# Kernel optimization log

Hardware: AMD Instinct MI355X
Metric: run time of the kernel (lower is better)

The kernel has to match this reference:

```python
import jax, jax.numpy as jnp
import numpy as np

# module config (matches init_kwargs)
EMBED = 128; HEADS = 8; HEAD_DIM = EMBED // HEADS  # 16, power of 2
MODES = 16            # hardcoded in FuncSelfAttention
WS = 4                # window_size
SHIFT = 2             # shift_size
NSUB = 8              # n_sub (subdomain grid of the full image)
NW = (NSUB // WS) ** 2   # 4 windows per image
S = WS * WS              # 16 tokens (subdomains) per window
BATCH0 = 4; B = BATCH0 * NW  # 16
P = 32                # per-subdomain spatial resolution (needs P//2+1 >= MODES)
HID = 512             # LogCPB MLP hidden width (Swin-v2 style)


def win_decompose2d(x, nsx, nsy, ws):
    # x: [b, c, H, W] -> [(b*wx*wy), ws*ws, c, sh, sw]
    b, c, H, W = x.shape
    sh = H // nsx; sw = W // nsy
    wx = nsx // ws; wy = nsy // ws
    x = x.reshape(b, c, wx, ws, sh, wy, ws, sw)
    x = x.transpose(0, 2, 5, 3, 6, 1, 4, 7)  # b, wx, wy, qx, qy, c, sh, sw
    return x.reshape(b * wx * wy, ws * ws, c, sh, sw)


def win_recompose2d(x, nsx, nsy, ws):
    # inverse of win_decompose2d: [(b*wx*wy), ws*ws, c, sh, sw] -> [b, c, H, W]
    wx = nsx // ws; wy = nsy // ws
    Bn, s, c, sh, sw = x.shape
    b = Bn // (wx * wy)
    x = x.reshape(b, wx, wy, ws, ws, c, sh, sw)
    x = x.transpose(0, 5, 1, 3, 6, 2, 4, 7)
    return x.reshape(b, c, wx * ws * sh, wy * ws * sw)


def spectral_conv(x, wr, wi):
    # SimpleSpectralConv2d: rfft2 -> low-mode complex channel mixing -> irfft2
    # x: [b, s, cin, h, w]; wr/wi: [cin, cout, m, m]
    m = wr.shape[-1]
    h, w = x.shape[-2:]
    xf = jnp.fft.rfft2(x, axes=(-2, -1))                       # [b,s,cin,h,w//2+1]
    ym = jnp.einsum('bsixy,ioxy->bsoxy', xf[..., :m, :m], wr + 1j * wi)
    out_ft = jnp.zeros(x.shape[:2] + (wr.shape[1], h, w // 2 + 1), dtype=ym.dtype)
    out_ft = out_ft.at[..., :m, :m].set(ym)
    return jnp.fft.irfft2(out_ft, s=(h, w), axes=(-2, -1))


def log_cpb(ws, w1, b1, w2):
    # Swin-v2 style log-spaced continuous position bias MLP -> [heads, S, S]
    g = jnp.arange(ws)
    coords = jnp.stack(jnp.meshgrid(g, g, indexing='ij'), -1).reshape(-1, 2)  # [S,2]
    rel = (coords[:, None, :] - coords[None, :, :]).astype(jnp.float32)       # [S,S,2]
    rel = jnp.sign(rel) * jnp.log2(1.0 + jnp.abs(rel)) / jnp.log2(8.0) * 8.0
    hdn = jax.nn.relu(rel @ w1 + b1)
    return (hdn @ w2).transpose(2, 0, 1)


def _build_attn_mask():
    # Faithful port of the Swin shifted-window mask construction in __init__
    img = np.zeros((NSUB, NSUB), np.float32)
    sl = [slice(0, -WS), slice(-WS, -SHIFT), slice(-SHIFT, None)]
    cnt = 0
    for hs in sl:
        for ws_ in sl:
            img[hs, ws_] = cnt
            cnt += 1
    mw = img.reshape(NSUB // WS, WS, NSUB // WS, WS).transpose(0, 2, 1, 3).reshape(NW, S)
    diff = mw[:, None, :] - mw[:, :, None]
    m = np.where(diff != 0, -1e9, 0.0).astype(np.float32)      # -inf in torch; -1e9 for safe grads
    return np.broadcast_to(m[:, None, :, :], (NW, HEADS, S, S)).copy()


def setup_inputs():
    key = jax.random.key(0)
    ks = jax.random.split(key, 8)
    sc = 1.0 / EMBED
    return {
        'seq': jax.random.normal(ks[0], (B, S, EMBED, P, P), jnp.float32),
        'qkv_wr': jax.random.normal(ks[1], (EMBED, 3 * EMBED, MODES, MODES), jnp.float32) * sc,
        'qkv_wi': jax.random.normal(ks[2], (EMBED, 3 * EMBED, MODES, MODES), jnp.float32) * sc,
        'out_wr': jax.random.normal(ks[3], (EMBED, EMBED, MODES, MODES), jnp.float32) * sc,
        'out_wi': jax.random.normal(ks[4], (EMBED, EMBED, MODES, MODES), jnp.float32) * sc,
        'cpb_w1': jax.random.normal(ks[5], (2, HID), jnp.float32) * 0.1,
        'cpb_b1': jnp.zeros((HID,), jnp.float32),
        'cpb_w2': jax.random.normal(ks[6], (HID, HEADS), jnp.float32) * 0.05,
        'attn_mask': jnp.asarray(_build_attn_mask()),
    }


def reference(seq, qkv_wr, qkv_wi, out_wr, out_wi, cpb_w1, cpb_b1, cpb_w2, attn_mask):
    Bn, s, C, h, w = seq.shape
    ssx = w // WS; ssy = h // WS  # subdomain_size per code: seq.size(-1)//n_sub_x with n_sub_x=window_size
    # shift: recompose windows to images, roll, decompose back
    x = win_recompose2d(seq, WS, WS, WS)
    x = jnp.roll(x, (-SHIFT * ssx, -SHIFT * ssy), axis=(-2, -1))
    x = win_decompose2d(x, WS, WS, WS)
    # qkv = spectral conv + residual tiling (v.repeat with dims[2]=3)
    qkv = spectral_conv(x, qkv_wr, qkv_wi) + jnp.concatenate([x, x, x], axis=2)
    qkv = qkv.reshape(Bn, s, 3, HEADS, HEAD_DIM, h, w)
    q = qkv[:, :, 0].transpose(0, 2, 1, 3, 4, 5)  # [B, H, s, d, h, w]
    k = qkv[:, :, 1].transpose(0, 2, 1, 3, 4, 5)
    v = qkv[:, :, 2].transpose(0, 2, 1, 3, 4, 5)
    bias = attn_mask + log_cpb(WS, cpb_w1, cpb_b1, cpb_w2)[None]  # [nW, H, S, S]
    # 'reimann' scores: Riemann-sum (mean over grid) inner product of q_i, k_j functions
    scale = 1.0 / ((h * w) * jnp.sqrt(jnp.float32(HEAD_DIM)))
    scores = jnp.einsum('bnidxy,bnjdxy->bnij', q, k) * scale      # [B, H, S, S]
    scores = scores.reshape(Bn // NW, NW, HEADS, s, s) + bias[None]
    attn = jax.nn.softmax(scores, axis=-1).reshape(Bn, HEADS, s, s)
    sa = jnp.einsum('bnij,bnjdxy->bnidxy', attn, v)               # [B, H, S, d, h, w]
    sa = sa.transpose(0, 2, 1, 3, 4, 5).reshape(Bn, s, C, h, w)   # _flatten
    sa = spectral_conv(sa, out_wr, out_wi)
    # un-shift
    sa = win_recompose2d(sa, WS, WS, WS)
    sa = jnp.roll(sa, (SHIFT * ssx, SHIFT * ssy), axis=(-2, -1))
    return win_decompose2d(sa, WS, WS, WS)
```

## Files before the change

### kernel.cpp

```cpp
#include <hip/hip_runtime.h>
#include <hip/hip_bf16.h>
#include <math.h>


#define DEVI __device__ __forceinline__
typedef unsigned short u16;
typedef unsigned int u32;
typedef __attribute__((ext_vector_type(8))) short short8;
typedef __attribute__((ext_vector_type(4))) float f32x4;

DEVI u16 f2b(float f) {
  union { __hip_bfloat16 h; u16 u; } cv;
  cv.h = __float2bfloat16(f);
  return cv.u;
}
DEVI float b2f(u16 u) { return __uint_as_float(((u32)u) << 16); }

__global__ __launch_bounds__(256) void k_bias(
    const float* __restrict__ w1, const float* __restrict__ b1,
    const float* __restrict__ w2, const float* __restrict__ amask,
    float* __restrict__ biasb) {
  __shared__ float w1s[1024];
  __shared__ float b1s[512];
  __shared__ float w2s[4096];
  int t = threadIdx.x;
  for (int k = t; k < 1024; k += 256) w1s[k] = w1[k];
  for (int k = t; k < 512; k += 256) b1s[k] = b1[k];
  for (int k = t; k < 4096; k += 256) w2s[k] = w2[k];
  __syncthreads();
  int i = t >> 4, j = t & 15;
  float r0 = (float)((i >> 2) - (j >> 2));
  float r1 = (float)((i & 3) - (j & 3));
  const float sc = 8.0f / 3.0f;
  float f0 = (r0 == 0.f) ? 0.f : copysignf(log2f(1.f + fabsf(r0)) * sc, r0);
  float f1 = (r1 == 0.f) ? 0.f : copysignf(log2f(1.f + fabsf(r1)) * sc, r1);
  float o[8];
#pragma unroll
  for (int h = 0; h < 8; h++) o[h] = 0.f;
  for (int k = 0; k < 512; k++) {
    float hd = f0 * w1s[k] + f1 * w1s[512 + k] + b1s[k];
    hd = fmaxf(hd, 0.f);
#pragma unroll
    for (int h = 0; h < 8; h++) o[h] += hd * w2s[k * 8 + h];
  }
  for (int w = 0; w < 4; w++)
#pragma unroll
    for (int h = 0; h < 8; h++) {
      int idx = ((w * 8 + h) * 16 + i) * 16 + j;
      biasb[idx] = amask[idx] + o[h];
    }
}

__global__ __launch_bounds__(256) void k_transpose_wb(
    const float* __restrict__ wr, const float* __restrict__ wi,
    ushort2* __restrict__ dst, int N) {
  __shared__ ushort2 ld[256][17];
  int t = threadIdx.x;
  int ob = blockIdx.x * 16;
  int cb = blockIdx.y * 8;
  for (int cc = 0; cc < 8; cc++) {
    int c = cb + cc;
    for (int oo = 0; oo < 16; oo++) {
      size_t si = ((size_t)c * N + ob + oo) * 256 + t;
      ushort2 u;
      u.x = f2b(wr[si]);
      u.y = f2b(wi[si]);
      ld[t][oo] = u;
    }
    __syncthreads();
    {
      int oo = t & 15, tq = t >> 4;
#pragma unroll
      for (int mr = 0; mr < 16; mr++) {
        int m = mr * 16 + tq;
        dst[((size_t)m * 128 + c) * N + ob + oo] = ld[m][oo];
      }
    }
    __syncthreads();
  }
}

template <int N>
__global__ __launch_bounds__(256) void k_build_b(
    const ushort2* __restrict__ Ws1, u16* __restrict__ Bt) {
  __shared__ ushort2 tile[128][65];
  int t = threadIdx.x;
  int ob = blockIdx.x;
  int m = blockIdx.y;
  {
    int c4 = t >> 6, o = t & 63;
    for (int cc = 0; cc < 32; cc++) {
      int c = cc * 4 + c4;
      tile[c][o] = Ws1[((size_t)m * 128 + c) * N + ob * 64 + o];
    }
  }
  __syncthreads();
  int l = t & 63, w2 = t >> 6;
  for (int rr = 0; rr < 32; rr++) {
    int r = w2 * 32 + rr;
    int ol = r >> 1, p = r & 1;
    size_t rowoff = ((size_t)m * (2 * N) + (size_t)ob * 128 + r) * 256;
#pragma unroll
    for (int ch = 0; ch < 2; ch++) {
      int c = ch * 64 + l;
      ushort2 wv = tile[c][ol];
      ushort2 u;
      u.x = p ? wv.y : wv.x;
      u.y = p ? wv.x : (u16)(wv.y ^ 0x8000);
      *(ushort2*)(Bt + rowoff + 2 * c) = u;
    }
  }
}

__global__ __launch_bounds__(256) void k_build_wdft(u16* __restrict__ Wdft) {
  int n = blockIdx.x;
  int m = n >> 1, q = n & 1;
  int kx = m >> 4, ky = m & 15;
  int t = threadIdx.x;
#pragma unroll
  for (int i = 0; i < 4; i++) {
    int p = i * 256 + t;
    int u = p >> 5, v = p & 31;
    int ph = (kx * u + ky * v) & 31;
    float th = 6.283185307179586f * (float)ph / 32.f;
    float sv, cv;
    sincosf(th, &sv, &cv);
    Wdft[(size_t)n * 1024 + p] = f2b(q ? -sv : cv);
  }
}

__global__ __launch_bounds__(256) void k_gather(
    const float* __restrict__ seq, u16* __restrict__ Tbf) {
  int t = threadIdx.x;
  int cq = blockIdx.x;
  int bs = blockIdx.y;
  int b = bs >> 4, s = bs & 15;
  int qx = s >> 2, qy = s & 3;
  int u = t >> 3, vb = (t & 7) * 4;
  int uu = u + 16;
  int u2 = uu & 31;
  int qx2 = (qx + (uu >> 5)) & 3;
  int vv = vb + 16;
  int v2 = vv & 31;
  int qy2 = (qy + (vv >> 5)) & 3;
  int s2 = qx2 * 4 + qy2;
  size_t srcbase = (((size_t)(b * 16 + s2) * 128) << 10) + u2 * 32 + v2;
  size_t dstbase = (((size_t)bs * 128) << 10) + u * 32 + vb;
  for (int cc = 0; cc < 32; cc++) {
    size_t coff = (size_t)(cq * 32 + cc) << 10;
    float4 v = *(const float4*)(seq + srcbase + coff);
    ushort4 o;
    o.x = f2b(v.x);
    o.y = f2b(v.y);
    o.z = f2b(v.z);
    o.w = f2b(v.w);
    *(ushort4*)(Tbf + dstbase + coff) = o;
  }
}

__global__ __launch_bounds__(512) void k_dftm(
    const u16* __restrict__ Wdft, const u16* __restrict__ Tbf,
    float2* __restrict__ Xlow, u16* __restrict__ Xbf) {
  __shared__ char As[32768];
  __shared__ char Bs[16384];
  int t = threadIdx.x;
  int mt = blockIdx.x, bs = blockIdx.y;
  int l = t & 63, w = t >> 6;
  int wm = w >> 1, wn = w & 1;
  f32x4 acc[4][4];
#pragma unroll
  for (int a_ = 0; a_ < 4; a_++)
#pragma unroll
    for (int b_ = 0; b_ < 4; b_++) acc[a_][b_] = (f32x4){0.f, 0.f, 0.f, 0.f};
  const u16* Ab = Wdft + (size_t)mt * 256 * 1024;
  const u16* Bb = Tbf + (size_t)bs * 128 * 1024;
  int srow = t >> 3, ss = t & 7;
  uint4 ra[4], rb[2];
#pragma unroll
  for (int i = 0; i < 4; i++)
    ra[i] = *(const uint4*)(Ab + (size_t)(i * 64 + srow) * 1024 + ss * 8);
#pragma unroll
  for (int i = 0; i < 2; i++)
    rb[i] = *(const uint4*)(Bb + (size_t)(i * 64 + srow) * 1024 + ss * 8);
  for (int kt = 0; kt < 16; kt++) {
    if (kt) __syncthreads();
#pragma unroll
    for (int i = 0; i < 4; i++) {
      int row = i * 64 + srow;
      *(uint4*)(As + row * 128 + ((ss ^ (row & 7)) << 4)) = ra[i];
    }
#pragma unroll
    for (int i = 0; i < 2; i++) {
      int row = i * 64 + srow;
      *(uint4*)(Bs + row * 128 + ((ss ^ (row & 7)) << 4)) = rb[i];
    }
    if (kt < 15) {
#pragma unroll
      for (int i = 0; i < 4; i++)
        ra[i] = *(const uint4*)(Ab + (size_t)(i * 64 + srow) * 1024 +
                                (kt + 1) * 64 + ss * 8);
#pragma unroll
      for (int i = 0; i < 2; i++)
        rb[i] = *(const uint4*)(Bb + (size_t)(i * 64 + srow) * 1024 +
                                (kt + 1) * 64 + ss * 8);
    }
    __syncthreads();
#pragma unroll
    for (int kk = 0; kk < 2; kk++) {
      short8 af[4], bg[4];
#pragma unroll
      for (int fm = 0; fm < 4; fm++) {
        int row = wm * 64 + fm * 16 + (l & 15);
        int chunk = kk * 4 + (l >> 4);
        af[fm] = *(const short8*)(As + row * 128 + ((chunk ^ (row & 7)) << 4));
      }
#pragma unroll
      for (int fn = 0; fn < 4; fn++) {
        int row = wn * 64 + fn * 16 + (l & 15);
        int chunk = kk * 4 + (l >> 4);
        bg[fn] = *(const short8*)(Bs + row * 128 + ((chunk ^ (row & 7)) << 4));
      }
#pragma unroll
      for (int fm = 0; fm < 4; fm++)
#pragma unroll
        for (int fn = 0; fn < 4; fn++)
          acc[fm][fn] = __builtin_amdgcn_mfma_f32_16x16x32_bf16(
              af[fm], bg[fn], acc[fm][fn], 0, 0, 0);
    }
  }
  int cr = (l >> 4) * 4, ccol = l & 15;
#pragma unroll
  for (int fm = 0; fm < 4; fm++) {
    int nbase = mt * 256 + wm * 64 + fm * 16 + cr;
#pragma unroll
    for (int fn = 0; fn < 4; fn++) {
      int c = wn * 64 + fn * 16 + ccol;
#pragma unroll
      for (int rp = 0; rp < 4; rp += 2) {
        int n0 = nbase + rp;
        size_t row = (size_t)(n0 >> 1) * 256 + bs;
        float v0 = acc[fm][fn][rp], v1 = acc[fm][fn][rp + 1];
        Xlow[row * 128 + c] = make_float2(v0, v1);
        ushort2 ub;
        ub.x = f2b(v0);
        ub.y = f2b(v1);
        *(ushort2*)(Xbf + row * 256 + 2 * c) = ub;
      }
    }
  }
}

__global__ __launch_bounds__(64) void k_gram_mfma(
    const u16* __restrict__ Tbf, float* __restrict__ Gpart) {
  int dc = blockIdx.x;
  int bh = blockIdx.y;
  int b = bh >> 3, h = bh & 7;
  int l = threadIdx.x;
  f32x4 a0 = (f32x4){0.f, 0.f, 0.f, 0.f};
  f32x4 a1 = (f32x4){0.f, 0.f, 0.f, 0.f};
  const u16* base =
      Tbf + ((size_t)(b * 16 + (l & 15)) * 128 + h * 16 + dc * 4) * 1024;
  int ko = (l >> 4) * 8;
  for (int kk = 0; kk < 128; kk += 2) {
    short8 f0 = *(const short8*)(base + kk * 32 + ko);
    short8 f1 = *(const short8*)(base + kk * 32 + 32 + ko);
    a0 = __builtin_amdgcn_mfma_f32_16x16x32_bf16(f0, f0, a0, 0, 0, 0);
    a1 = __builtin_amdgcn_mfma_f32_16x16x32_bf16(f1, f1, a1, 0, 0, 0);
  }
  float* dst = Gpart + ((size_t)(dc * 16 + b) * 8 + h) * 256;
#pragma unroll
  for (int r = 0; r < 4; r++)
    dst[((l >> 4) * 4 + r) * 16 + (l & 15)] = a0[r] + a1[r];
}

template <int NP, bool OUTBF>
__global__ __launch_bounds__(512) void k_mixm(
    const u16* __restrict__ A, const u16* __restrict__ Bm,
    float* __restrict__ Cf, u16* __restrict__ Cb) {
  __shared__ char lds[65536];
  char* As = lds;
  char* Bs = lds + 32768;
  int t = threadIdx.x;
  const int gx = NP / 256;
  int orig = blockIdx.y * gx + blockIdx.x;
  const int tot = gx * 256;
  int lid = (orig & 7) * (tot >> 3) + (orig >> 3);
  int nt = lid % gx;
  int m = lid / gx;
  int l = t & 63, w = t >> 6;
  int wm = w >> 1, wn = w & 1;
  f32x4 acc[4][8];
#pragma unroll
  for (int a_ = 0; a_ < 4; a_++)
#pragma unroll
    for (int b_ = 0; b_ < 8; b_++) acc[a_][b_] = (f32x4){0.f, 0.f, 0.f, 0.f};
  const u16* Ab = A + (size_t)m * 256 * 256;
  const u16* Bb = Bm + ((size_t)m * NP + nt * 256) * 256;
  int srow = t >> 3, ss = t & 7;
  uint4 ra[4], rb[4];
#pragma unroll
  for (int i = 0; i < 4; i++) {
    int row = i * 64 + srow;
    ra[i] = *(const uint4*)(Ab + (size_t)row * 256 + ss * 8);
    rb[i] = *(const uint4*)(Bb + (size_t)row * 256 + ss * 8);
  }
  for (int kt = 0; kt < 4; kt++) {
    if (kt) __syncthreads();
#pragma unroll
    for (int i = 0; i < 4; i++) {
      int row = i * 64 + srow;
      int sw = ((ss ^ (row & 7)) << 4);
      *(uint4*)(As + row * 128 + sw) = ra[i];
      *(uint4*)(Bs + row * 128 + sw) = rb[i];
    }
    if (kt < 3) {
#pragma unroll
      for (int i = 0; i < 4; i++) {
        int row = i * 64 + srow;
        ra[i] =
            *(const uint4*)(Ab + (size_t)row * 256 + (kt + 1) * 64 + ss * 8);
        rb[i] =
            *(const uint4*)(Bb + (size_t)row * 256 + (kt + 1) * 64 + ss * 8);
      }
    }
    __syncthreads();
#pragma unroll
    for (int kk = 0; kk < 2; kk++) {
      short8 af[4], bg[8];
#pragma unroll
      for (int fm = 0; fm < 4; fm++) {
        int row = wm * 64 + fm * 16 + (l & 15);
        int chunk = kk * 4 + (l >> 4);
        af[fm] = *(const short8*)(As + row * 128 + ((chunk ^ (row & 7)) << 4));
      }
#pragma unroll
      for (int fn = 0; fn < 8; fn++) {
        int row = wn * 128 + fn * 16 + (l & 15);
        int chunk = kk * 4 + (l >> 4);
        bg[fn] = *(const short8*)(Bs + row * 128 + ((chunk ^ (row & 7)) << 4));
      }
#pragma unroll
      for (int fm = 0; fm < 4; fm++)
#pragma unroll
        for (int fn = 0; fn < 8; fn++)
          acc[fm][fn] = __builtin_amdgcn_mfma_f32_16x16x32_bf16(
              bg[fn], af[fm], acc[fm][fn], 0, 0, 0);
    }
  }
#pragma unroll
  for (int fm = 0; fm < 4; fm++) {
    int bs = wm * 64 + fm * 16 + (l & 15);
    size_t rowbase = ((size_t)m * 256 + bs) * NP + nt * 256;
#pragma unroll
    for (int fn = 0; fn < 8; fn++) {
      int n0 = wn * 128 + fn * 16 + (l >> 4) * 4;
      if (OUTBF) {
        ushort4 u;
        u.x = f2b(acc[fm][fn][0]);
        u.y = f2b(acc[fm][fn][1]);
        u.z = f2b(acc[fm][fn][2]);
        u.w = f2b(acc[fm][fn][3]);
        *(ushort4*)(Cb + rowbase + n0) = u;
      } else {
        *(float4*)(Cf + rowbase + n0) = make_float4(
            acc[fm][fn][0], acc[fm][fn][1], acc[fm][fn][2], acc[fm][fn][3]);
      }
    }
  }
}

__global__ __launch_bounds__(256) void k_scores(
    const float2* __restrict__ Xlow, const ushort2* __restrict__ QKVmb,
    float* __restrict__ Spart) {
  __shared__ float2 Xs[16][17], Qs[16][17], Ks[16][17];
  int t = threadIdx.x;
  int mc = blockIdx.x;
  int bh = blockIdx.y;
  int b = bh >> 3, h = bh & 7;
  int i = t >> 4, j = t & 15;
  int bs = b * 16 + i;
  int d = j;
  int m0 = mc * 32;
  size_t xoff = ((size_t)m0 * 256 + bs) * 128 + h * 16 + d;
  size_t qoff = ((size_t)m0 * 256 + bs) * 384 + h * 16 + d;
  float2 px = Xlow[xoff];
  ushort2 uq = QKVmb[qoff];
  ushort2 uk = QKVmb[qoff + 128];
  float acc = 0.f;
  for (int mm = 0; mm < 32; mm++) {
    int m = m0 + mm;
    Xs[i][d] = px;
    Qs[i][d] = make_float2(b2f(uq.x), b2f(uq.y));
    Ks[i][d] = make_float2(b2f(uk.x), b2f(uk.y));
    __syncthreads();
    if (mm < 31) {
      px = Xlow[xoff + (size_t)(mm + 1) * 32768];
      uq = QKVmb[qoff + (size_t)(mm + 1) * 98304];
      uk = QKVmb[qoff + (size_t)(mm + 1) * 98304 + 128];
    }
    int ky = m & 15, kx = m >> 4;
    if (ky > 0) {
#pragma unroll
      for (int dd = 0; dd < 16; dd++) {
        float2 Xi = Xs[i][dd], Qi = Qs[i][dd], Xj = Xs[j][dd], Kj = Ks[j][dd];
        float qr = Xi.x + Qi.x, qi = Xi.y + Qi.y;
        float kr = Xj.x + Kj.x, ki = Xj.y + Kj.y;
        acc += 2.f * (qr * kr + qi * ki - (Xi.x * Xj.x + Xi.y * Xj.y));
      }
    } else {
#pragma unroll
      for (int dd = 0; dd < 16; dd++) {
        float2 Xi = Xs[i][dd], Qi = Qs[i][dd], Xj = Xs[j][dd], Kj = Ks[j][dd];
        float cr = Xi.x * Kj.x + Xi.y * Kj.y + Qi.x * Xj.x + Qi.y * Xj.y;
        float qk =
            (kx == 0) ? (Qi.x * Kj.x) : 0.5f * (Qi.x * Kj.x + Qi.y * Kj.y);
        acc += cr + qk;
      }
    }
    __syncthreads();
  }
  Spart[((size_t)mc * 128 + bh) * 256 + t] = acc;
}

__global__ __launch_bounds__(256) void k_softmax(
    const float* __restrict__ Spart, const float* __restrict__ Gpart,
    const float* __restrict__ biasb, float* __restrict__ attn) {
  int t = threadIdx.x;
  int bh = blockIdx.x;
  int b = bh >> 3, h = bh & 7;
  int i = t >> 4, j = t & 15;
  float acc = 0.f;
#pragma unroll
  for (int mc = 0; mc < 8; mc++)
    acc += Spart[((size_t)mc * 128 + bh) * 256 + t];
  float G = 0.f;
#pragma unroll
  for (int dc = 0; dc < 4; dc++)
    G += Gpart[((size_t)(dc * 16 + b) * 8 + h) * 256 + t];
  float score = G * (1.f / 4096.f) + acc * (1.f / 4194304.f) +
                biasb[(((b & 3) * 8 + h) * 16 + i) * 16 + j];
  float mx = score;
#pragma unroll
  for (int o = 8; o >= 1; o >>= 1) mx = fmaxf(mx, __shfl_xor(mx, o, 16));
  float e = expf(score - mx);
  float sm = e;
#pragma unroll
  for (int o = 8; o >= 1; o >>= 1) sm += __shfl_xor(sm, o, 16);
  attn[(size_t)bh * 256 + t] = e / sm;
}

__global__ __launch_bounds__(256) void k_sav(
    const float2* __restrict__ Xlow, const ushort2* __restrict__ QKVmb,
    const float* __restrict__ attn, ushort2* __restrict__ SAfb) {
  __shared__ float at[8][16][17];
  __shared__ float2 vt[16][130];
  int t = threadIdx.x;
  int mc = blockIdx.x;
  int b = blockIdx.y;
  {
    int h = t >> 5, ii = (t >> 1) & 15, jb = (t & 1) * 8;
#pragma unroll
    for (int k = 0; k < 8; k++)
      at[h][ii][jb + k] = attn[((size_t)(b * 8 + h) * 16 + ii) * 16 + jb + k];
  }
  __syncthreads();
  int i = t >> 4, cg = t & 15;
  for (int mm = 0; mm < 16; mm++) {
    int m = mc * 16 + mm;
    int ky = m & 15, kx = m >> 4;
    {
      int jj = t >> 4;
      size_t row = (size_t)m * 256 + b * 16 + jj;
#pragma unroll
      for (int u = 0; u < 8; u++) {
        int c = cg + u * 16;
        ushort2 uv = QKVmb[row * 384 + 256 + c];
        float2 vm = make_float2(b2f(uv.x), b2f(uv.y));
        float2 xv = Xlow[row * 128 + c];
        float2 vh;
        if (ky == 0) {
          if (kx == 0)
            vh = make_float2(xv.x + vm.x, xv.y);
          else
            vh = make_float2(xv.x + 0.5f * vm.x, xv.y + 0.5f * vm.y);
        } else
          vh = make_float2(xv.x + vm.x, xv.y + vm.y);
        vt[jj][c] = vh;
      }
    }
    __syncthreads();
    float2 o8[8];
#pragma unroll
    for (int u = 0; u < 8; u++) o8[u] = make_float2(0.f, 0.f);
#pragma unroll
    for (int jj = 0; jj < 16; jj++) {
#pragma unroll
      for (int u = 0; u < 8; u++) {
        float av = at[u][i][jj];
        float2 v = vt[jj][cg + u * 16];
        o8[u].x += av * v.x;
        o8[u].y += av * v.y;
      }
    }
    size_t orow = (size_t)m * 256 + b * 16 + i;
#pragma unroll
    for (int u = 0; u < 8; u++) {
      ushort2 ub;
      ub.x = f2b(o8[u].x);
      ub.y = f2b(o8[u].y);
      SAfb[orow * 128 + cg + u * 16] = ub;
    }
    __syncthreads();
  }
}

__global__ __launch_bounds__(256) void k_irfft_out(
    const float2* __restrict__ OUTm, float* __restrict__ out) {
  __shared__ float2 Fm[256][17];
  __shared__ float2 gb[17][33];
  __shared__ float2 tw[32];
  int t = threadIdx.x;
  int oc = blockIdx.x;
  int bs = blockIdx.y;
  int b = bs >> 4, s = bs & 15;
  int qx = s >> 2, qy = s & 3;
  if (t < 32) {
    float sv, cv;
    sincosf(6.283185307179586f * (float)t / 32.f, &sv, &cv);
    tw[t] = make_float2(cv, sv);
  }
  {
    const float2* src = &OUTm[((size_t)t * 256 + bs) * 128 + oc * 16];
#pragma unroll
    for (int oo = 0; oo < 16; oo++) Fm[t][oo] = src[oo];
  }
  __syncthreads();
  for (int oo = 0; oo < 16; oo++) {
    {
      int x = t >> 3, kp = t & 7;
#pragma unroll
      for (int q = 0; q < 2; q++) {
        int ky = kp * 2 + q;
        float gr = 0.f, gi = 0.f;
#pragma unroll
        for (int kx = 0; kx < 16; kx++) {
          float2 F = Fm[kx * 16 + ky][oo];
          float2 w = tw[(kx * x) & 31];
          gr += F.x * w.x - F.y * w.y;
          gi += F.x * w.y + F.y * w.x;
        }
        gb[ky][x] = make_float2(gr, gi);
      }
    }
    __syncthreads();
    {
      int x = t >> 3, yb = (t & 7) * 4;
      float vals[4];
#pragma unroll
      for (int k = 0; k < 4; k++) {
        int y = yb + k;
        float v = gb[0][x].x;
#pragma unroll
        for (int ky = 1; ky < 16; ky++) {
          float2 g = gb[ky][x];
          float2 w = tw[(ky * y) & 31];
          v += 2.f * (g.x * w.x - g.y * w.y);
        }
        vals[k] = v * (1.f / 1024.f);
      }
      int uu = x + 16;
      int u2 = uu & 31;
      int qx2 = (qx + (uu >> 5)) & 3;
      int vv = yb + 16;
      int v2 = vv & 31;
      int qy2 = (qy + (vv >> 5)) & 3;
      int s2 = qx2 * 4 + qy2;
      int o_abs = oc * 16 + oo;
      float* dst = &out[(((size_t)(b * 16 + s2) * 128 + o_abs) << 10) +
                        (u2 << 5) + v2];
      *(float4*)dst = make_float4(vals[0], vals[1], vals[2], vals[3]);
    }
    __syncthreads();
  }
}

extern "C" void kernel_launch(void* const* d_in, const int* in_sizes, int n_in,
                              void* d_out, int out_size, void* d_ws,
                              size_t ws_size, hipStream_t stream) {
  (void)in_sizes;
  (void)n_in;
  const float* seq = (const float*)d_in[0];
  const float* qwr = (const float*)d_in[1];
  const float* qwi = (const float*)d_in[2];
  const float* owr = (const float*)d_in[3];
  const float* owi = (const float*)d_in[4];
  const float* cw1 = (const float*)d_in[5];
  const float* cb1 = (const float*)d_in[6];
  const float* cw2 = (const float*)d_in[7];
  const float* amask = (const float*)d_in[8];
  float* out = (float*)d_out;
  char* ws = (char*)d_ws;

  const size_t R = 100663296;
  ushort2* Wq_s1b = (ushort2*)ws;
  u16* Tbf = (u16*)ws;
  u16* Xbf = (u16*)(ws + 67108864);
  u16* Wob = (u16*)ws;
  ushort2* QKVmb = (ushort2*)(ws + R);
  float2* OUTm = (float2*)(ws + R);
  u16* Wqb = (u16*)(ws + 2 * R);
  ushort2* SAfb = (ushort2*)(ws + 2 * R);
  ushort2* Wo_s1b = (ushort2*)(ws + 3 * R);
  float2* Xlow = (float2*)(ws + 3 * R + 16777216);
  char* sm = ws + 3 * R + 16777216 + 67108864;
  u16* Wdft = (u16*)sm;
  float* Gpart = (float*)(sm + 1048576);
  float* biasb = (float*)(sm + 1572864);
  float* attn = (float*)(sm + 1605632);
  float* Spart = (float*)(sm + 1736704);
  size_t need = 3 * R + 16777216 + 67108864 + 2785280;

  if (ws_size < need) {
    hipMemsetAsync(d_out, 0, (size_t)out_size * 4, stream);
    return;
  }

  dim3 blk(256);
  k_transpose_wb<<<dim3(24, 16), blk, 0, stream>>>(qwr, qwi, Wq_s1b, 384);
  k_build_b<384><<<dim3(6, 256), blk, 0, stream>>>(Wq_s1b, Wqb);
  k_transpose_wb<<<dim3(8, 16), blk, 0, stream>>>(owr, owi, Wo_s1b, 128);
  k_bias<<<dim3(1), blk, 0, stream>>>(cw1, cb1, cw2, amask, biasb);
  k_build_wdft<<<dim3(512), blk, 0, stream>>>(Wdft);
  k_gather<<<dim3(4, 256), blk, 0, stream>>>(seq, Tbf);
  k_dftm<<<dim3(2, 256), dim3(512), 0, stream>>>(Wdft, Tbf, Xlow, Xbf);
  k_gram_mfma<<<dim3(4, 128), dim3(64), 0, stream>>>(Tbf, Gpart);
  k_mixm<768, true><<<dim3(3, 256), dim3(512), 0, stream>>>(
      Xbf, Wqb, (float*)nullptr, (u16*)QKVmb);
  k_scores<<<dim3(8, 128), blk, 0, stream>>>(Xlow, QKVmb, Spart);
  k_softmax<<<dim3(128), blk, 0, stream>>>(Spart, Gpart, biasb, attn);
  k_build_b<128><<<dim3(2, 256), blk, 0, stream>>>(Wo_s1b, Wob);
  k_sav<<<dim3(16, 16), blk, 0, stream>>>(Xlow, QKVmb, attn, SAfb);
  k_mixm<256, false><<<dim3(1, 256), dim3(512), 0, stream>>>(
      (const u16*)SAfb, Wob, (float*)OUTm, (u16*)nullptr);
  k_irfft_out<<<dim3(8, 256), blk, 0, stream>>>(OUTm, out);
}
```

Baseline: 787.8 us.

## Replace scalar inverse DFT output stage with bf16 MFMA GEMM against precomputed IDFT matrix

Replaces the scalar two-stage inverse real FFT kernel with a dense bf16 MFMA GEMM. The GEMM multiplies a precomputed inverse-DFT basis matrix (with the real-FFT doubling weights folded in) by the spectral output. The output-mixing GEMM now emits bf16, and a new transpose kernel lays out the modes contiguously per subdomain and channel for the GEMM. The change moves the inverse transform onto matrix cores but adds a transpose pass, an extra workspace buffer, and bf16 rounding of the spectral output and basis.

```diff
diff --git a/kernel.cpp b/kernel.cpp
--- a/kernel.cpp
+++ b/kernel.cpp
@@ -126,6 +126,21 @@
     float sv, cv;
     sincosf(th, &sv, &cv);
     Wdft[(size_t)n * 1024 + p] = f2b(q ? -sv : cv);
+  }
+}
+
+__global__ __launch_bounds__(256) void k_build_widft(u16* __restrict__ Widf) {
+  int p = blockIdx.x;
+  int x = p >> 5, y = p & 31;
+  for (int n = threadIdx.x; n < 512; n += 256) {
+    int m = n >> 1, q = n & 1;
+    int kx = m >> 4, ky = m & 15;
+    int ph = (kx * x + ky * y) & 31;
+    float th = 6.283185307179586f * (float)ph / 32.f;
+    float sv, cv;
+    sincosf(th, &sv, &cv);
+    float cky = (ky == 0) ? (1.f / 1024.f) : (2.f / 1024.f);
+    Widf[(size_t)p * 512 + n] = f2b(q ? -sv * cky : cv * cky);
   }
 }
 
@@ -369,6 +384,126 @@
   }
 }
 
+__global__ __launch_bounds__(256) void k_transp_out(
+    const ushort2* __restrict__ OUTb2, ushort2* __restrict__ OUTt2) {
+  __shared__ ushort2 ld[128][129];
+  int t = threadIdx.x;
+  int bs = blockIdx.x;
+  for (int mh = 0; mh < 2; mh++) {
+    if (mh) __syncthreads();
+    {
+      int cidx = t & 127;
+      int rb = t >> 7;
+      for (int pass = 0; pass < 64; pass++) {
+        int r = pass * 2 + rb;
+        ld[r][cidx] = OUTb2[((size_t)(mh * 128 + r) * 256 + bs) * 128 + cidx];
+      }
+    }
+    __syncthreads();
+    {
+      int ml = t & 127;
+      int cb = t >> 7;
+      for (int pass = 0; pass < 64; pass++) {
+        int c = pass * 2 + cb;
+        OUTt2[((size_t)bs * 128 + c) * 256 + mh * 128 + ml] = ld[ml][c];
+      }
+    }
+  }
+}
+
+__global__ __launch_bounds__(512) void k_irfftm(
+    const u16* __restrict__ Widf, const u16* __restrict__ OUTt,
+    float* __restrict__ out) {
+  __shared__ char As[32768];
+  __shared__ char Bs[16384];
+  int t = threadIdx.x;
+  int ph = blockIdx.x, bs = blockIdx.y;
+  int b = bs >> 4, s = bs & 15;
+  int qx = s >> 2, qy = s & 3;
+  int l = t & 63, w = t >> 6;
+  int wm = w >> 1, wn = w & 1;
+  f32x4 acc[4][4];
+#pragma unroll
+  for (int a_ = 0; a_ < 4; a_++)
+#pragma unroll
+    for (int b_ = 0; b_ < 4; b_++) acc[a_][b_] = (f32x4){0.f, 0.f, 0.f, 0.f};
+  const u16* Ab = Widf + (size_t)ph * 256 * 512;
+  const u16* Bb = OUTt + (size_t)bs * 128 * 512;
+  int srow = t >> 3, ss = t & 7;
+  uint4 ra[4], rb[2];
+#pragma unroll
+  for (int i = 0; i < 4; i++)
+    ra[i] = *(const uint4*)(Ab + (size_t)(i * 64 + srow) * 512 + ss * 8);
+#pragma unroll
+  for (int i = 0; i < 2; i++)
+    rb[i] = *(const uint4*)(Bb + (size_t)(i * 64 + srow) * 512 + ss * 8);
+  for (int kt = 0; kt < 8; kt++) {
+    if (kt) __syncthreads();
+#pragma unroll
+    for (int i = 0; i < 4; i++) {
+      int row = i * 64 + srow;
+      *(uint4*)(As + row * 128 + ((ss ^ (row & 7)) << 4)) = ra[i];
+    }
+#pragma unroll
+    for (int i = 0; i < 2; i++) {
+      int row = i * 64 + srow;
+      *(uint4*)(Bs + row * 128 + ((ss ^ (row & 7)) << 4)) = rb[i];
+    }
+    if (kt < 7) {
+#pragma unroll
+      for (int i = 0; i < 4; i++)
+        ra[i] = *(const uint4*)(Ab + (size_t)(i * 64 + srow) * 512 +
+                                (kt + 1) * 64 + ss * 8);
+#pragma unroll
+      for (int i = 0; i < 2; i++)
+        rb[i] = *(const uint4*)(Bb + (size_t)(i * 64 + srow) * 512 +
+                                (kt + 1) * 64 + ss * 8);
+    }
+    __syncthreads();
+#pragma unroll
+    for (int kk = 0; kk < 2; kk++) {
+      short8 wf[4], bg[4];
+#pragma unroll
+      for (int fm = 0; fm < 4; fm++) {
+        int row = wm * 64 + fm * 16 + (l & 15);
+        int chunk = kk * 4 + (l >> 4);
+        wf[fm] = *(const short8*)(As + row * 128 + ((chunk ^ (row & 7)) << 4));
+      }
+#pragma unroll
+      for (int fn = 0; fn < 4; fn++) {
+        int row = wn * 64 + fn * 16 + (l & 15);
+        int chunk = kk * 4 + (l >> 4);
+        bg[fn] = *(const short8*)(Bs + row * 128 + ((chunk ^ (row & 7)) << 4));
+      }
+#pragma unroll
+      for (int fm = 0; fm < 4; fm++)
+#pragma unroll
+        for (int fn = 0; fn < 4; fn++)
+          acc[fm][fn] = __builtin_amdgcn_mfma_f32_16x16x32_bf16(
+              wf[fm], bg[fn], acc[fm][fn], 0, 0, 0);
+    }
+  }
+#pragma unroll
+  for (int fm = 0; fm < 4; fm++) {
+    int pg = ph * 256 + wm * 64 + fm * 16 + (l >> 4) * 4;
+    int x = pg >> 5, yb = pg & 31;
+    int uu = x + 16;
+    int u2 = uu & 31;
+    int qx2 = (qx + (uu >> 5)) & 3;
+    int vv = yb + 16;
+    int v2 = vv & 31;
+    int qy2 = (qy + (vv >> 5)) & 3;
+    int s2 = qx2 * 4 + qy2;
+    size_t obase = (((size_t)(b * 16 + s2) * 128) << 10) + u2 * 32 + v2;
+#pragma unroll
+    for (int fn = 0; fn < 4; fn++) {
+      int c = wn * 64 + fn * 16 + (l & 15);
+      *(float4*)(out + obase + ((size_t)c << 10)) = make_float4(
+          acc[fm][fn][0], acc[fm][fn][1], acc[fm][fn][2], acc[fm][fn][3]);
+    }
+  }
+}
+
 __global__ __launch_bounds__(256) void k_scores(
     const float2* __restrict__ Xlow, const ushort2* __restrict__ QKVmb,
     float* __restrict__ Spart) {
@@ -514,76 +649,6 @@
   }
 }
 
-__global__ __launch_bounds__(256) void k_irfft_out(
-    const float2* __restrict__ OUTm, float* __restrict__ out) {
-  __shared__ float2 Fm[256][17];
-  __shared__ float2 gb[17][33];
-  __shared__ float2 tw[32];
-  int t = threadIdx.x;
-  int oc = blockIdx.x;
-  int bs = blockIdx.y;
-  int b = bs >> 4, s = bs & 15;
-  int qx = s >> 2, qy = s & 3;
-  if (t < 32) {
-    float sv, cv;
-    sincosf(6.283185307179586f * (float)t / 32.f, &sv, &cv);
-    tw[t] = make_float2(cv, sv);
-  }
-  {
-    const float2* src = &OUTm[((size_t)t * 256 + bs) * 128 + oc * 16];
-#pragma unroll
-    for (int oo = 0; oo < 16; oo++) Fm[t][oo] = src[oo];
-  }
-  __syncthreads();
-  for (int oo = 0; oo < 16; oo++) {
-    {
-      int x = t >> 3, kp = t & 7;
-#pragma unroll
-      for (int q = 0; q < 2; q++) {
-        int ky = kp * 2 + q;
-        float gr = 0.f, gi = 0.f;
-#pragma unroll
-        for (int kx = 0; kx < 16; kx++) {
-          float2 F = Fm[kx * 16 + ky][oo];
-          float2 w = tw[(kx * x) & 31];
-          gr += F.x * w.x - F.y * w.y;
-          gi += F.x * w.y + F.y * w.x;
-        }
-        gb[ky][x] = make_float2(gr, gi);
-      }
-    }
-    __syncthreads();
-    {
-      int x = t >> 3, yb = (t & 7) * 4;
-      float vals[4];
-#pragma unroll
-      for (int k = 0; k < 4; k++) {
-        int y = yb + k;
-        float v = gb[0][x].x;
-#pragma unroll
-        for (int ky = 1; ky < 16; ky++) {
-          float2 g = gb[ky][x];
-          float2 w = tw[(ky * y) & 31];
-          v += 2.f * (g.x * w.x - g.y * w.y);
-        }
-        vals[k] = v * (1.f / 1024.f);
-      }
-      int uu = x + 16;
-      int u2 = uu & 31;
-      int qx2 = (qx + (uu >> 5)) & 3;
-      int vv = yb + 16;
-      int v2 = vv & 31;
-      int qy2 = (qy + (vv >> 5)) & 3;
-      int s2 = qx2 * 4 + qy2;
-      int o_abs = oc * 16 + oo;
-      float* dst = &out[(((size_t)(b * 16 + s2) * 128 + o_abs) << 10) +
-                        (u2 << 5) + v2];
-      *(float4*)dst = make_float4(vals[0], vals[1], vals[2], vals[3]);
-    }
-    __syncthreads();
-  }
-}
-
 extern "C" void kernel_launch(void* const* d_in, const int* in_sizes, int n_in,
                               void* d_out, int out_size, void* d_ws,
                               size_t ws_size, hipStream_t stream) {
@@ -607,7 +672,8 @@
   u16* Xbf = (u16*)(ws + 67108864);
   u16* Wob = (u16*)ws;
   ushort2* QKVmb = (ushort2*)(ws + R);
-  float2* OUTm = (float2*)(ws + R);
+  u16* OUTb = (u16*)(ws + R);
+  u16* OUTt = (u16*)(ws + R + 33554432);
   u16* Wqb = (u16*)(ws + 2 * R);
   ushort2* SAfb = (ushort2*)(ws + 2 * R);
   ushort2* Wo_s1b = (ushort2*)(ws + 3 * R);
@@ -618,7 +684,8 @@
   float* biasb = (float*)(sm + 1572864);
   float* attn = (float*)(sm + 1605632);
   float* Spart = (float*)(sm + 1736704);
-  size_t need = 3 * R + 16777216 + 67108864 + 2785280;
+  u16* Widf = (u16*)(sm + 2785280);
+  size_t need = 3 * R + 16777216 + 67108864 + 2785280 + 1048576;
 
   if (ws_size < need) {
     hipMemsetAsync(d_out, 0, (size_t)out_size * 4, stream);
@@ -631,6 +698,7 @@
   k_transpose_wb<<<dim3(8, 16), blk, 0, stream>>>(owr, owi, Wo_s1b, 128);
   k_bias<<<dim3(1), blk, 0, stream>>>(cw1, cb1, cw2, amask, biasb);
   k_build_wdft<<<dim3(512), blk, 0, stream>>>(Wdft);
+  k_build_widft<<<dim3(1024), blk, 0, stream>>>(Widf);
   k_gather<<<dim3(4, 256), blk, 0, stream>>>(seq, Tbf);
   k_dftm<<<dim3(2, 256), dim3(512), 0, stream>>>(Wdft, Tbf, Xlow, Xbf);
   k_gram_mfma<<<dim3(4, 128), dim3(64), 0, stream>>>(Tbf, Gpart);
@@ -640,7 +708,9 @@
   k_softmax<<<dim3(128), blk, 0, stream>>>(Spart, Gpart, biasb, attn);
   k_build_b<128><<<dim3(2, 256), blk, 0, stream>>>(Wo_s1b, Wob);
   k_sav<<<dim3(16, 16), blk, 0, stream>>>(Xlow, QKVmb, attn, SAfb);
-  k_mixm<256, false><<<dim3(1, 256), dim3(512), 0, stream>>>(
-      (const u16*)SAfb, Wob, (float*)OUTm, (u16*)nullptr);
-  k_irfft_out<<<dim3(8, 256), blk, 0, stream>>>(OUTm, out);
-}
+  k_mixm<256, true><<<dim3(1, 256), dim3(512), 0, stream>>>(
+      (const u16*)SAfb, Wob, (float*)nullptr, OUTb);
+  k_transp_out<<<dim3(256), blk, 0, stream>>>((const ushort2*)OUTb,
+                                              (ushort2*)OUTt);
+  k_irfftm<<<dim3(4, 256), dim3(512), 0, stream>>>(Widf, OUTt, out);
+}
```

Result: slower. 819.8 us (+4.1%).
